# Performance work log

Measured on AMD Instinct MI355X. Metric: run time of the kernel, lower is better.

The kernel has to match this reference:

```python
import jax, jax.numpy as jnp
import numpy as np

EMBED_DIM = 1024
NUM_HEADS = 16
HEAD_DIM = EMBED_DIM // NUM_HEADS
SCALE = HEAD_DIM ** -0.5


def setup_inputs() -> dict:
    key = jax.random.key(0)
    ks = jax.random.split(key, 9)
    B, N = 2, 2048
    s = EMBED_DIM ** -0.5  # ~ torch Linear init scale
    x = jax.random.normal(ks[0], (B, N, EMBED_DIM), dtype=jnp.float32)
    Wq = jax.random.uniform(ks[1], (EMBED_DIM, EMBED_DIM), jnp.float32, -s, s)
    bq = jax.random.uniform(ks[2], (EMBED_DIM,), jnp.float32, -s, s)
    Wk = jax.random.uniform(ks[3], (EMBED_DIM, EMBED_DIM), jnp.float32, -s, s)
    bk = jax.random.uniform(ks[4], (EMBED_DIM,), jnp.float32, -s, s)
    Wv = jax.random.uniform(ks[5], (EMBED_DIM, EMBED_DIM), jnp.float32, -s, s)
    bv = jax.random.uniform(ks[6], (EMBED_DIM,), jnp.float32, -s, s)
    Wo = jax.random.uniform(ks[7], (EMBED_DIM, EMBED_DIM), jnp.float32, -s, s)
    bo = jax.random.uniform(ks[8], (EMBED_DIM,), jnp.float32, -s, s)
    return {"x": x, "Wq": Wq, "bq": bq, "Wk": Wk, "bk": bk,
            "Wv": Wv, "bv": bv, "Wo": Wo, "bo": bo}


def reference(x, Wq, bq, Wk, bk, Wv, bv, Wo, bo):
    B, N, R = x.shape
    H, D = NUM_HEADS, HEAD_DIM
    # projections: Linear(x) = x @ W^T + b; reshape to (B, H, N, D)
    def proj(W, b):
        return (x @ W.T + b).reshape(B, N, H, D).transpose(0, 2, 1, 3)
    q = proj(Wq, bq)
    k = proj(Wk, bk)
    v = proj(Wv, bv)
    attn = jnp.einsum('bhnd,bhmd->bhnm', q, k) * SCALE  # (B,H,N,N)
    attn = jax.nn.softmax(attn, axis=-1)
    out = jnp.einsum('bhnm,bhmd->bhnd', attn, v)        # (B,H,N,D)
    out = out.transpose(0, 2, 1, 3).reshape(B, N, R)
    return out @ Wo.T + bo
```

## Files before the change

kernel.cpp:

```cpp
#include <hip/hip_runtime.h>
#include <stdint.h>

typedef __bf16 bf16;
typedef __bf16 bf16x4 __attribute__((ext_vector_type(4)));
typedef __bf16 bf16x8 __attribute__((ext_vector_type(8)));
typedef float f32x4 __attribute__((ext_vector_type(4)));

#define MFMA16(a, b, c) __builtin_amdgcn_mfma_f32_16x16x32_bf16((a), (b), (c), 0, 0, 0)

#define EMBED 1024
#define SEQ   2048
#define MROWS 4096
#define ATTN_QSCALE 0.1803368801111f

__device__ __forceinline__ void gl2lds16(const bf16* g, bf16* l) {
    __builtin_amdgcn_global_load_lds(
        (const __attribute__((address_space(1))) void*)g,
        (__attribute__((address_space(3))) void*)l,
        16, 0, 0);
}

__global__ __launch_bounds__(256) void cast_all_kernel(
    const float* __restrict__ x,  const float* __restrict__ Wq,
    const float* __restrict__ Wk, const float* __restrict__ Wv,
    const float* __restrict__ Wo, bf16* __restrict__ dst) {
    const int blk = blockIdx.x;
    const float* src;
    size_t so, dofs;
    if (blk < 2048) {
        src = x; so = (size_t)blk * 2048; dofs = so;
    } else {
        const int w = (blk - 2048) >> 9;
        so  = (size_t)((blk - 2048) & 511) * 2048;
        src = (w == 0) ? Wq : (w == 1) ? Wk : (w == 2) ? Wv : Wo;
        dofs = (size_t)(4 + w) * 1024 * 1024 + so;
    }
    const size_t i = (size_t)threadIdx.x * 8;
    float4 a = *(const float4*)(src + so + i);
    float4 b = *(const float4*)(src + so + i + 4);
    bf16x8 o;
    o[0] = (bf16)a.x; o[1] = (bf16)a.y; o[2] = (bf16)a.z; o[3] = (bf16)a.w;
    o[4] = (bf16)b.x; o[5] = (bf16)b.y; o[6] = (bf16)b.z; o[7] = (bf16)b.w;
    *(bf16x8*)(dst + dofs + i) = o;
}

template <bool SCALE>
__device__ __forceinline__ void gemm_tile(const bf16* __restrict__ A,
                                          const bf16* __restrict__ W,
                                          const float* __restrict__ bias,
                                          bf16* __restrict__ C,
                                          int m0, int n0, bf16* smem) {
    const int lane = threadIdx.x & 63;
    const int wv   = threadIdx.x >> 6;
    const int wm   = (wv >> 1) * 64;
    const int wn   = (wv & 1) * 64;
    const int fr   = lane & 15;
    const int quad = lane >> 4;
    const int srow = wv * 8 + (lane >> 3);
    const int swz  = (((lane & 7) ^ ((lane >> 3) & 7))) * 8;

    f32x4 acc[4][4];
#pragma unroll
    for (int mt = 0; mt < 4; ++mt)
#pragma unroll
        for (int nt = 0; nt < 4; ++nt)
            acc[mt][nt] = (f32x4){0.f, 0.f, 0.f, 0.f};

    auto stage = [&](int kt, int bb) {
        bf16* As = smem + bb * 16384;
        bf16* Bs = As + 8192;
        const int k0 = kt * 64;
#pragma unroll
        for (int i = 0; i < 4; ++i) {
            gl2lds16(A + (size_t)(m0 + i * 32 + srow) * 1024 + k0 + swz,
                     &As[(i * 32 + wv * 8) * 64]);
            gl2lds16(W + (size_t)(n0 + i * 32 + srow) * 1024 + k0 + swz,
                     &Bs[(i * 32 + wv * 8) * 64]);
        }
    };

    stage(0, 0);
#pragma unroll
    for (int kt = 0; kt < 16; ++kt) {
        const int bb = kt & 1;
        asm volatile("s_waitcnt vmcnt(0)" ::: "memory");
        __builtin_amdgcn_s_barrier();
        if (kt < 15) stage(kt + 1, bb ^ 1);
        const bf16* As = smem + bb * 16384;
        const bf16* Bs = As + 8192;
#pragma unroll
        for (int ks = 0; ks < 2; ++ks) {
            const int fcol = ((ks * 4 + quad) ^ (fr & 7)) * 8;
            bf16x8 af[4], bfr[4];
#pragma unroll
            for (int t = 0; t < 4; ++t) {
                af[t]  = *(const bf16x8*)&As[(wm + t * 16 + fr) * 64 + fcol];
                bfr[t] = *(const bf16x8*)&Bs[(wn + t * 16 + fr) * 64 + fcol];
            }
            __builtin_amdgcn_s_setprio(1);
#pragma unroll
            for (int mt = 0; mt < 4; ++mt)
#pragma unroll
                for (int nt = 0; nt < 4; ++nt)
                    acc[mt][nt] = MFMA16(af[mt], bfr[nt], acc[mt][nt]);
            __builtin_amdgcn_s_setprio(0);
        }
    }

    float bv[4];
#pragma unroll
    for (int nt = 0; nt < 4; ++nt)
        bv[nt] = bias[n0 + wn + nt * 16 + fr];
    const int row4 = quad * 4;
#pragma unroll
    for (int mt = 0; mt < 4; ++mt)
#pragma unroll
        for (int nt = 0; nt < 4; ++nt)
#pragma unroll
            for (int r = 0; r < 4; ++r) {
                int m = m0 + wm + mt * 16 + row4 + r;
                int n = n0 + wn + nt * 16 + fr;
                float v = acc[mt][nt][r] + bv[nt];
                if (SCALE) v *= ATTN_QSCALE;
                C[(size_t)m * 1024 + n] = (bf16)v;
            }
}

__device__ __forceinline__ void v_tile(const bf16* __restrict__ x,
                                       const bf16* __restrict__ Wv,
                                       const float* __restrict__ bias,
                                       bf16* __restrict__ VT,
                                       int m0, int n0, bf16* smem) {
    const int lane = threadIdx.x & 63;
    const int wv   = threadIdx.x >> 6;
    const int wmW  = (wv >> 1) * 64;
    const int wnT  = (wv & 1) * 64;
    const int f    = lane & 15;
    const int quad = lane >> 4;
    const int srow = wv * 8 + (lane >> 3);
    const int swz  = (((lane & 7) ^ ((lane >> 3) & 7))) * 8;

    f32x4 acc[4][4];
#pragma unroll
    for (int mt = 0; mt < 4; ++mt)
#pragma unroll
        for (int nt = 0; nt < 4; ++nt)
            acc[mt][nt] = (f32x4){0.f, 0.f, 0.f, 0.f};

    auto stage = [&](int kt, int bb) {
        bf16* As = smem + bb * 16384;
        bf16* Bs = As + 8192;
        const int k0 = kt * 64;
#pragma unroll
        for (int i = 0; i < 4; ++i) {
            gl2lds16(x  + (size_t)(m0 + i * 32 + srow) * 1024 + k0 + swz,
                     &As[(i * 32 + wv * 8) * 64]);
            gl2lds16(Wv + (size_t)(n0 + i * 32 + srow) * 1024 + k0 + swz,
                     &Bs[(i * 32 + wv * 8) * 64]);
        }
    };

    stage(0, 0);
#pragma unroll
    for (int kt = 0; kt < 16; ++kt) {
        const int bb = kt & 1;
        asm volatile("s_waitcnt vmcnt(0)" ::: "memory");
        __builtin_amdgcn_s_barrier();
        if (kt < 15) stage(kt + 1, bb ^ 1);
        const bf16* As = smem + bb * 16384;
        const bf16* Bs = As + 8192;
#pragma unroll
        for (int ks = 0; ks < 2; ++ks) {
            const int fcol = ((ks * 4 + quad) ^ (f & 7)) * 8;
            bf16x8 wf[4], xf[4];
#pragma unroll
            for (int t = 0; t < 4; ++t) {
                wf[t] = *(const bf16x8*)&Bs[(wmW + t * 16 + f) * 64 + fcol];
                xf[t] = *(const bf16x8*)&As[(wnT + t * 16 + f) * 64 + fcol];
            }
            __builtin_amdgcn_s_setprio(1);
#pragma unroll
            for (int mt = 0; mt < 4; ++mt)
#pragma unroll
                for (int nt = 0; nt < 4; ++nt)
                    acc[mt][nt] = MFMA16(wf[mt], xf[nt], acc[mt][nt]);
            __builtin_amdgcn_s_setprio(0);
        }
    }

    float4 b4[4];
#pragma unroll
    for (int mt = 0; mt < 4; ++mt)
        b4[mt] = *(const float4*)&bias[n0 + wmW + mt * 16 + quad * 4];

    __syncthreads();

#pragma unroll
    for (int mt = 0; mt < 4; ++mt)
#pragma unroll
        for (int nt = 0; nt < 4; ++nt) {
            const int tok = wnT + nt * 16 + f;
#pragma unroll
            for (int r = 0; r < 4; ++r) {
                const float bvr = (r == 0) ? b4[mt].x : (r == 1) ? b4[mt].y
                                : (r == 2) ? b4[mt].z : b4[mt].w;
                smem[(wmW + mt * 16 + quad * 4 + r) * 136 + tok] =
                    (bf16)(acc[mt][nt][r] + bvr);
            }
        }
    __syncthreads();

    const int n_r  = threadIdx.x >> 4;
    const int t8   = (threadIdx.x & 15) * 8;
    const int base = t8 & ~31;
    const int u4   = ((t8 >> 3) & 3) * 4;
    const int bb   = m0 >> 11;
    const int tokg = (m0 & 2047) + t8;
#pragma unroll
    for (int p = 0; p < 8; ++p) {
        const int n_loc = p * 16 + n_r;
        const bf16* row = &smem[n_loc * 136];
        bf16x4 a = *(const bf16x4*)&row[base + u4];
        bf16x4 b = *(const bf16x4*)&row[base + 16 + u4];
        bf16x8 v = {a[0], a[1], a[2], a[3], b[0], b[1], b[2], b[3]};
        *(bf16x8*)&VT[((size_t)(bb * 1024 + n0 + n_loc)) * 2048 + tokg] = v;
    }
}

__global__ __launch_bounds__(256) void qkv_kernel(
    const bf16* __restrict__ x,
    const bf16* __restrict__ Wq, const float* __restrict__ bq,
    const bf16* __restrict__ Wk, const float* __restrict__ bk,
    const bf16* __restrict__ Wv, const float* __restrict__ bv,
    bf16* __restrict__ Q, bf16* __restrict__ K, bf16* __restrict__ VT) {
    __shared__ __align__(16) bf16 smem[32768];
    const int m0    = blockIdx.x * 128;
    const int which = blockIdx.y >> 3;
    const int n0    = (blockIdx.y & 7) * 128;
    if (which == 0)      gemm_tile<true>(x, Wq, bq, Q, m0, n0, smem);
    else if (which == 1) gemm_tile<false>(x, Wk, bk, K, m0, n0, smem);
    else                 v_tile(x, Wv, bv, VT, m0, n0, smem);
}

__global__ __launch_bounds__(256) void oproj_kernel(
    const bf16* __restrict__ A, const bf16* __restrict__ W,
    const float* __restrict__ bias, float* __restrict__ C) {
    const int m0 = blockIdx.x * 128;
    const int n0 = blockIdx.y * 64;

    __shared__ __align__(16) bf16 smem[24576];

    const int lane = threadIdx.x & 63;
    const int wv   = threadIdx.x >> 6;
    const int wm   = (wv >> 1) * 64;
    const int wn   = (wv & 1) * 32;
    const int fr   = lane & 15;
    const int quad = lane >> 4;
    const int srow = wv * 8 + (lane >> 3);
    const int swz  = (((lane & 7) ^ ((lane >> 3) & 7))) * 8;

    f32x4 acc[4][2];
#pragma unroll
    for (int mt = 0; mt < 4; ++mt)
#pragma unroll
        for (int nt = 0; nt < 2; ++nt)
            acc[mt][nt] = (f32x4){0.f, 0.f, 0.f, 0.f};

    auto stage = [&](int kt, int bb) {
        bf16* As = smem + bb * 12288;
        bf16* Bs = As + 8192;
        const int k0 = kt * 64;
#pragma unroll
        for (int i = 0; i < 4; ++i)
            gl2lds16(A + (size_t)(m0 + i * 32 + srow) * 1024 + k0 + swz,
                     &As[(i * 32 + wv * 8) * 64]);
#pragma unroll
        for (int i = 0; i < 2; ++i)
            gl2lds16(W + (size_t)(n0 + i * 32 + srow) * 1024 + k0 + swz,
                     &Bs[(i * 32 + wv * 8) * 64]);
    };

    stage(0, 0);
#pragma unroll
    for (int kt = 0; kt < 16; ++kt) {
        const int bb = kt & 1;
        asm volatile("s_waitcnt vmcnt(0)" ::: "memory");
        __builtin_amdgcn_s_barrier();
        if (kt < 15) stage(kt + 1, bb ^ 1);
        const bf16* As = smem + bb * 12288;
        const bf16* Bs = As + 8192;
#pragma unroll
        for (int ks = 0; ks < 2; ++ks) {
            const int fcol = ((ks * 4 + quad) ^ (fr & 7)) * 8;
            bf16x8 af[4], bfr[2];
#pragma unroll
            for (int t = 0; t < 4; ++t)
                af[t] = *(const bf16x8*)&As[(wm + t * 16 + fr) * 64 + fcol];
#pragma unroll
            for (int t = 0; t < 2; ++t)
                bfr[t] = *(const bf16x8*)&Bs[(wn + t * 16 + fr) * 64 + fcol];
            __builtin_amdgcn_s_setprio(1);
#pragma unroll
            for (int mt = 0; mt < 4; ++mt)
#pragma unroll
                for (int nt = 0; nt < 2; ++nt)
                    acc[mt][nt] = MFMA16(af[mt], bfr[nt], acc[mt][nt]);
            __builtin_amdgcn_s_setprio(0);
        }
    }

    float bv[2];
#pragma unroll
    for (int nt = 0; nt < 2; ++nt)
        bv[nt] = bias[n0 + wn + nt * 16 + fr];
    const int row4 = quad * 4;
#pragma unroll
    for (int mt = 0; mt < 4; ++mt)
#pragma unroll
        for (int nt = 0; nt < 2; ++nt)
#pragma unroll
            for (int r = 0; r < 4; ++r) {
                int m = m0 + wm + mt * 16 + row4 + r;
                int n = n0 + wn + nt * 16 + fr;
                C[(size_t)m * 1024 + n] = acc[mt][nt][r] + bv[nt];
            }
}

__global__ __launch_bounds__(256, 2) void attn_kernel(
    const bf16* __restrict__ Q, const bf16* __restrict__ K,
    const bf16* __restrict__ VT, bf16* __restrict__ Opart,
    float* __restrict__ lpart) {
    const int tid  = threadIdx.x;
    const int lane = tid & 63;
    const int wv   = tid >> 6;
    const int quad = lane >> 4;
    const int f    = lane & 15;
    const int lin  = blockIdx.y * 16 + blockIdx.x;
    const int sw   = (lin & 7) * 64 + (lin >> 3);
    const int qh   = sw & 15;
    const int bh   = sw >> 4;
    const int qt   = qh >> 1;
    const int half = qh & 1;
    const int q0   = qt * 256;
    const int kvb  = half * 1024;
    const int b    = bh >> 4;
    const int h    = bh & 15;

    const bf16* Qp = Q + ((size_t)b * SEQ) * 1024 + (size_t)h * 64;
    const bf16* Kp = K + ((size_t)b * SEQ) * 1024 + (size_t)h * 64;
    const bf16* Vp = VT + ((size_t)(b * 1024 + h * 64)) * 2048;
    bf16*  Op = Opart + (size_t)half * MROWS * 1024
                      + ((size_t)b * SEQ) * 1024 + (size_t)h * 64;
    float* lp = lpart + ((size_t)(half * 2 + b) * 16 + h) * SEQ;

    __shared__ bf16 Ks[4][64 * 64];
    __shared__ bf16 VTs[4][64 * 64];

    bf16x8 qf[4][2];
#pragma unroll
    for (int qg = 0; qg < 4; ++qg) {
        const bf16* qrow = Qp + (size_t)(q0 + wv * 64 + qg * 16 + f) * 1024;
        qf[qg][0] = *(const bf16x8*)(qrow + quad * 8);
        qf[qg][1] = *(const bf16x8*)(qrow + 32 + quad * 8);
    }

    const int srow = wv * 8 + (lane >> 3);
    const int swz  = (((lane & 7) ^ ((lane >> 3) & 7))) * 8;
    auto stageK = [&](int t, int bb) {
        const int kv0 = kvb + t * 64;
#pragma unroll
        for (int i = 0; i < 2; ++i)
            gl2lds16(Kp + (size_t)(kv0 + i * 32 + srow) * 1024 + swz,
                     &Ks[bb][(i * 32 + wv * 8) * 64]);
    };
    auto stageVT = [&](int t, int bb) {
        const int kv0 = kvb + t * 64;
#pragma unroll
        for (int i = 0; i < 2; ++i)
            gl2lds16(Vp + (size_t)(i * 32 + srow) * 2048 + kv0 + swz,
                     &VTs[bb][(i * 32 + wv * 8) * 64]);
    };

    stageK(0, 0); stageVT(0, 0);
    stageK(1, 1); stageVT(1, 1);

    f32x4 oacc[4][4];
#pragma unroll
    for (int qg = 0; qg < 4; ++qg)
#pragma unroll
        for (int t = 0; t < 4; ++t)
            oacc[qg][t] = (f32x4){0.f, 0.f, 0.f, 0.f};
    f32x4 lacc[4];
#pragma unroll
    for (int qg = 0; qg < 4; ++qg)
        lacc[qg] = (f32x4){0.f, 0.f, 0.f, 0.f};
    const bf16x8 ones8 = {(bf16)1.f, (bf16)1.f, (bf16)1.f, (bf16)1.f,
                          (bf16)1.f, (bf16)1.f, (bf16)1.f, (bf16)1.f};
    const f32x4  zero4 = (f32x4){0.f, 0.f, 0.f, 0.f};

    const int fcol0 = (quad ^ (f & 7)) * 8;
    const int fcol1 = ((4 + quad) ^ (f & 7)) * 8;

    bf16x8 pbA[4][2], pbB[4][2];

    asm volatile("s_waitcnt vmcnt(4)" ::: "memory");
    __builtin_amdgcn_s_barrier();
    {
        bf16x8 kf0[4], kf1[4];
#pragma unroll
        for (int t4 = 0; t4 < 4; ++t4) {
            kf0[t4] = *(const bf16x8*)&Ks[0][(t4 * 16 + f) * 64 + fcol0];
            kf1[t4] = *(const bf16x8*)&Ks[0][(t4 * 16 + f) * 64 + fcol1];
        }
#pragma unroll
        for (int qg = 0; qg < 4; ++qg) {
            f32x4 s[4];
            __builtin_amdgcn_s_setprio(1);
#pragma unroll
            for (int t4 = 0; t4 < 4; ++t4) {
                s[t4] = MFMA16(kf0[t4], qf[qg][0], zero4);
                s[t4] = MFMA16(kf1[t4], qf[qg][1], s[t4]);
            }
            __builtin_amdgcn_s_setprio(0);
#pragma unroll
            for (int kt = 0; kt < 2; ++kt) {
#pragma unroll
                for (int r = 0; r < 4; ++r) {
                    pbA[qg][kt][r]     = (bf16)__builtin_amdgcn_exp2f(s[2 * kt][r]);
                    pbA[qg][kt][4 + r] = (bf16)__builtin_amdgcn_exp2f(s[2 * kt + 1][r]);
                }
                lacc[qg] = MFMA16(ones8, pbA[qg][kt], lacc[qg]);
            }
        }
    }

    auto step = [&](int t, bf16x8 (&pbc)[4][2], bf16x8 (&pbn)[4][2],
                    int drain, bool doStage, bool doQK) {
        if (doStage) { stageK(t + 2, (t + 2) & 3); stageVT(t + 2, (t + 2) & 3); }
        if (drain == 4) asm volatile("s_waitcnt vmcnt(4)" ::: "memory");
        else            asm volatile("s_waitcnt vmcnt(0)" ::: "memory");
        __builtin_amdgcn_s_barrier();
        const int bq = (t + 1) & 3;
        const int bp = t & 3;

        bf16x8 kf0[4], kf1[4];
        if (doQK) {
#pragma unroll
            for (int t4 = 0; t4 < 4; ++t4) {
                kf0[t4] = *(const bf16x8*)&Ks[bq][(t4 * 16 + f) * 64 + fcol0];
                kf1[t4] = *(const bf16x8*)&Ks[bq][(t4 * 16 + f) * 64 + fcol1];
            }
        }
#pragma unroll
        for (int u = 0; u < 4; ++u) {
            f32x4 s[4];
            if (doQK) {
                __builtin_amdgcn_s_setprio(1);
#pragma unroll
                for (int t4 = 0; t4 < 4; ++t4) {
                    s[t4] = MFMA16(kf0[t4], qf[u][0], zero4);
                    s[t4] = MFMA16(kf1[t4], qf[u][1], s[t4]);
                }
                __builtin_amdgcn_s_setprio(0);
            }
            __builtin_amdgcn_s_setprio(1);
#pragma unroll
            for (int kt = 0; kt < 2; ++kt) {
                const int pc = ((kt * 4 + quad) ^ (f & 7)) * 8;
                bf16x8 vf = *(const bf16x8*)&VTs[bp][(u * 16 + f) * 64 + pc];
#pragma unroll
                for (int qg = 0; qg < 4; ++qg)
                    oacc[qg][u] = MFMA16(vf, pbc[qg][kt], oacc[qg][u]);
            }
            __builtin_amdgcn_s_setprio(0);
            if (doQK) {
#pragma unroll
                for (int kt = 0; kt < 2; ++kt) {
#pragma unroll
                    for (int r = 0; r < 4; ++r) {
                        pbn[u][kt][r]     = (bf16)__builtin_amdgcn_exp2f(s[2 * kt][r]);
                        pbn[u][kt][4 + r] = (bf16)__builtin_amdgcn_exp2f(s[2 * kt + 1][r]);
                    }
                    lacc[u] = MFMA16(ones8, pbn[u][kt], lacc[u]);
                }
            }
        }
    };

    for (int tt = 0; tt < 14; tt += 2) {
        step(tt,     pbA, pbB, 4, true, true);
        step(tt + 1, pbB, pbA, 4, true, true);
    }
    step(14, pbA, pbB, 0, false, true);
    step(15, pbB, pbA, 0, false, false);

#pragma unroll
    for (int qg = 0; qg < 4; ++qg) {
        const int q = q0 + wv * 64 + qg * 16 + f;
        bf16* orow = Op + (size_t)q * 1024;
#pragma unroll
        for (int dt = 0; dt < 4; ++dt) {
            bf16x4 ov;
#pragma unroll
            for (int r = 0; r < 4; ++r)
                ov[r] = (bf16)oacc[qg][dt][r];
            *(bf16x4*)(orow + dt * 16 + quad * 4) = ov;
        }
        if (quad == 0)
            lp[q] = lacc[qg][0];
    }
}

__global__ __launch_bounds__(256) void combine_kernel(
    const bf16* __restrict__ Opart, const float* __restrict__ lpart,
    bf16* __restrict__ O) {
    const int gid = blockIdx.x * 256 + threadIdx.x;
    const int row = gid >> 7;
    const int c8  = (gid & 127) * 8;
    const int b   = row >> 11;
    const int tok = row & 2047;
    const int h   = c8 >> 6;

    const float l = lpart[((size_t)(0 * 2 + b) * 16 + h) * SEQ + tok]
                  + lpart[((size_t)(1 * 2 + b) * 16 + h) * SEQ + tok];
    const float inv = 1.0f / l;

    const size_t off = (size_t)row * 1024 + c8;
    bf16x8 a = *(const bf16x8*)&Opart[off];
    bf16x8 c = *(const bf16x8*)&Opart[(size_t)MROWS * 1024 + off];
    bf16x8 o;
#pragma unroll
    for (int i = 0; i < 8; ++i)
        o[i] = (bf16)(((float)a[i] + (float)c[i]) * inv);
    *(bf16x8*)&O[off] = o;
}

extern "C" void kernel_launch(void* const* d_in, const int* in_sizes, int n_in,
                              void* d_out, int out_size, void* d_ws, size_t ws_size,
                              hipStream_t stream) {
    const float* x  = (const float*)d_in[0];
    const float* Wq = (const float*)d_in[1];
    const float* bq = (const float*)d_in[2];
    const float* Wk = (const float*)d_in[3];
    const float* bk = (const float*)d_in[4];
    const float* Wv = (const float*)d_in[5];
    const float* bv = (const float*)d_in[6];
    const float* Wo = (const float*)d_in[7];
    const float* bo = (const float*)d_in[8];
    float* out = (float*)d_out;

    bf16* xb    = (bf16*)d_ws;
    bf16* Wqb   = xb   + (size_t)MROWS * 1024;
    bf16* Wkb   = Wqb  + (size_t)1024 * 1024;
    bf16* Wvb   = Wkb  + (size_t)1024 * 1024;
    bf16* Wob   = Wvb  + (size_t)1024 * 1024;
    bf16* Q     = Wob  + (size_t)1024 * 1024;
    bf16* K     = Q    + (size_t)MROWS * 1024;
    bf16* VT    = K    + (size_t)MROWS * 1024;
    bf16* O     = VT   + (size_t)MROWS * 1024;
    bf16* Opart = O    + (size_t)MROWS * 1024;
    float* lpart = (float*)(Opart + (size_t)2 * MROWS * 1024);

    cast_all_kernel<<<4096, 256, 0, stream>>>(x, Wq, Wk, Wv, Wo, xb);

    qkv_kernel<<<dim3(32, 24), 256, 0, stream>>>(xb, Wqb, bq, Wkb, bk, Wvb, bv, Q, K, VT);
    attn_kernel<<<dim3(16, 32), 256, 0, stream>>>(Q, K, VT, Opart, lpart);
    combine_kernel<<<2048, 256, 0, stream>>>(Opart, lpart, O);
    oproj_kernel<<<dim3(32, 16), 256, 0, stream>>>(O, Wob, bo, out);
}
```

Baseline: 175.8 us.

## Switch projection GEMMs to triple-buffered K=32 stages with partial vmcnt waits

The QKV and output-projection GEMMs now stage K in chunks of 32 instead of 64, using a three-slot LDS ring that is prefetched two stages ahead. Waits use a partial vmcnt, so the next stage's loads stay in flight while the current one is consumed, instead of draining all loads each iteration. LDS per block drops, which may allow more resident blocks. The cost is twice as many barriers, and less MFMA work between them, and the XOR swizzle is narrowed to four 16-byte chunks, which may raise LDS bank conflicts.

New measurement: 180.0 us. 1.02x slower.

```diff
diff --git a/kernel.cpp b/kernel.cpp
--- a/kernel.cpp
+++ b/kernel.cpp
@@ -56,8 +56,9 @@
     const int wn   = (wv & 1) * 64;
     const int fr   = lane & 15;
     const int quad = lane >> 4;
-    const int srow = wv * 8 + (lane >> 3);
-    const int swz  = (((lane & 7) ^ ((lane >> 3) & 7))) * 8;
+    const int srow = wv * 16 + (lane >> 2);
+    const int swz  = ((lane & 3) ^ ((lane >> 2) & 3)) * 8;
+    const int fcol = (quad ^ (fr & 3)) * 8;
 
     f32x4 acc[4][4];
 #pragma unroll
@@ -67,44 +68,41 @@
             acc[mt][nt] = (f32x4){0.f, 0.f, 0.f, 0.f};
 
     auto stage = [&](int kt, int bb) {
-        bf16* As = smem + bb * 16384;
-        bf16* Bs = As + 8192;
-        const int k0 = kt * 64;
-#pragma unroll
-        for (int i = 0; i < 4; ++i) {
-            gl2lds16(A + (size_t)(m0 + i * 32 + srow) * 1024 + k0 + swz,
-                     &As[(i * 32 + wv * 8) * 64]);
-            gl2lds16(W + (size_t)(n0 + i * 32 + srow) * 1024 + k0 + swz,
-                     &Bs[(i * 32 + wv * 8) * 64]);
+        bf16* As = smem + bb * 8192;
+        bf16* Bs = As + 4096;
+        const int k0 = kt * 32;
+#pragma unroll
+        for (int c = 0; c < 2; ++c) {
+            gl2lds16(A + (size_t)(m0 + c * 64 + srow) * 1024 + k0 + swz,
+                     &As[(c * 64 + wv * 16) * 32]);
+            gl2lds16(W + (size_t)(n0 + c * 64 + srow) * 1024 + k0 + swz,
+                     &Bs[(c * 64 + wv * 16) * 32]);
         }
     };
 
     stage(0, 0);
-#pragma unroll
-    for (int kt = 0; kt < 16; ++kt) {
-        const int bb = kt & 1;
-        asm volatile("s_waitcnt vmcnt(0)" ::: "memory");
+    stage(1, 1);
+#pragma unroll
+    for (int kt = 0; kt < 32; ++kt) {
+        if (kt < 31) asm volatile("s_waitcnt vmcnt(4)" ::: "memory");
+        else         asm volatile("s_waitcnt vmcnt(0)" ::: "memory");
         __builtin_amdgcn_s_barrier();
-        if (kt < 15) stage(kt + 1, bb ^ 1);
-        const bf16* As = smem + bb * 16384;
-        const bf16* Bs = As + 8192;
-#pragma unroll
-        for (int ks = 0; ks < 2; ++ks) {
-            const int fcol = ((ks * 4 + quad) ^ (fr & 7)) * 8;
-            bf16x8 af[4], bfr[4];
-#pragma unroll
-            for (int t = 0; t < 4; ++t) {
-                af[t]  = *(const bf16x8*)&As[(wm + t * 16 + fr) * 64 + fcol];
-                bfr[t] = *(const bf16x8*)&Bs[(wn + t * 16 + fr) * 64 + fcol];
-            }
-            __builtin_amdgcn_s_setprio(1);
-#pragma unroll
-            for (int mt = 0; mt < 4; ++mt)
-#pragma unroll
-                for (int nt = 0; nt < 4; ++nt)
-                    acc[mt][nt] = MFMA16(af[mt], bfr[nt], acc[mt][nt]);
-            __builtin_amdgcn_s_setprio(0);
-        }
+        if (kt < 30) stage(kt + 2, (kt + 2) % 3);
+        const bf16* As = smem + (kt % 3) * 8192;
+        const bf16* Bs = As + 4096;
+        bf16x8 af[4], bfr[4];
+#pragma unroll
+        for (int t = 0; t < 4; ++t) {
+            af[t]  = *(const bf16x8*)&As[(wm + t * 16 + fr) * 32 + fcol];
+            bfr[t] = *(const bf16x8*)&Bs[(wn + t * 16 + fr) * 32 + fcol];
+        }
+        __builtin_amdgcn_s_setprio(1);
+#pragma unroll
+        for (int mt = 0; mt < 4; ++mt)
+#pragma unroll
+            for (int nt = 0; nt < 4; ++nt)
+                acc[mt][nt] = MFMA16(af[mt], bfr[nt], acc[mt][nt]);
+        __builtin_amdgcn_s_setprio(0);
     }
 
     float bv[4];
@@ -137,8 +135,9 @@
     const int wnT  = (wv & 1) * 64;
     const int f    = lane & 15;
     const int quad = lane >> 4;
-    const int srow = wv * 8 + (lane >> 3);
-    const int swz  = (((lane & 7) ^ ((lane >> 3) & 7))) * 8;
+    const int srow = wv * 16 + (lane >> 2);
+    const int swz  = ((lane & 3) ^ ((lane >> 2) & 3)) * 8;
+    const int fcol = (quad ^ (f & 3)) * 8;
 
     f32x4 acc[4][4];
 #pragma unroll
@@ -148,44 +147,41 @@
             acc[mt][nt] = (f32x4){0.f, 0.f, 0.f, 0.f};
 
     auto stage = [&](int kt, int bb) {
-        bf16* As = smem + bb * 16384;
-        bf16* Bs = As + 8192;
-        const int k0 = kt * 64;
-#pragma unroll
-        for (int i = 0; i < 4; ++i) {
-            gl2lds16(x  + (size_t)(m0 + i * 32 + srow) * 1024 + k0 + swz,
-                     &As[(i * 32 + wv * 8) * 64]);
-            gl2lds16(Wv + (size_t)(n0 + i * 32 + srow) * 1024 + k0 + swz,
-                     &Bs[(i * 32 + wv * 8) * 64]);
+        bf16* As = smem + bb * 8192;
+        bf16* Bs = As + 4096;
+        const int k0 = kt * 32;
+#pragma unroll
+        for (int c = 0; c < 2; ++c) {
+            gl2lds16(x  + (size_t)(m0 + c * 64 + srow) * 1024 + k0 + swz,
+                     &As[(c * 64 + wv * 16) * 32]);
+            gl2lds16(Wv + (size_t)(n0 + c * 64 + srow) * 1024 + k0 + swz,
+                     &Bs[(c * 64 + wv * 16) * 32]);
         }
     };
 
     stage(0, 0);
-#pragma unroll
-    for (int kt = 0; kt < 16; ++kt) {
-        const int bb = kt & 1;
-        asm volatile("s_waitcnt vmcnt(0)" ::: "memory");
+    stage(1, 1);
+#pragma unroll
+    for (int kt = 0; kt < 32; ++kt) {
+        if (kt < 31) asm volatile("s_waitcnt vmcnt(4)" ::: "memory");
+        else         asm volatile("s_waitcnt vmcnt(0)" ::: "memory");
         __builtin_amdgcn_s_barrier();
-        if (kt < 15) stage(kt + 1, bb ^ 1);
-        const bf16* As = smem + bb * 16384;
-        const bf16* Bs = As + 8192;
-#pragma unroll
-        for (int ks = 0; ks < 2; ++ks) {
-            const int fcol = ((ks * 4 + quad) ^ (f & 7)) * 8;
-            bf16x8 wf[4], xf[4];
-#pragma unroll
-            for (int t = 0; t < 4; ++t) {
-                wf[t] = *(const bf16x8*)&Bs[(wmW + t * 16 + f) * 64 + fcol];
-                xf[t] = *(const bf16x8*)&As[(wnT + t * 16 + f) * 64 + fcol];
-            }
-            __builtin_amdgcn_s_setprio(1);
-#pragma unroll
-            for (int mt = 0; mt < 4; ++mt)
-#pragma unroll
-                for (int nt = 0; nt < 4; ++nt)
-                    acc[mt][nt] = MFMA16(wf[mt], xf[nt], acc[mt][nt]);
-            __builtin_amdgcn_s_setprio(0);
-        }
+        if (kt < 30) stage(kt + 2, (kt + 2) % 3);
+        const bf16* As = smem + (kt % 3) * 8192;
+        const bf16* Bs = As + 4096;
+        bf16x8 wf[4], xf[4];
+#pragma unroll
+        for (int t = 0; t < 4; ++t) {
+            wf[t] = *(const bf16x8*)&Bs[(wmW + t * 16 + f) * 32 + fcol];
+            xf[t] = *(const bf16x8*)&As[(wnT + t * 16 + f) * 32 + fcol];
+        }
+        __builtin_amdgcn_s_setprio(1);
+#pragma unroll
+        for (int mt = 0; mt < 4; ++mt)
+#pragma unroll
+            for (int nt = 0; nt < 4; ++nt)
+                acc[mt][nt] = MFMA16(wf[mt], xf[nt], acc[mt][nt]);
+        __builtin_amdgcn_s_setprio(0);
     }
 
     float4 b4[4];
@@ -233,7 +229,7 @@
     const bf16* __restrict__ Wk, const float* __restrict__ bk,
     const bf16* __restrict__ Wv, const float* __restrict__ bv,
     bf16* __restrict__ Q, bf16* __restrict__ K, bf16* __restrict__ VT) {
-    __shared__ __align__(16) bf16 smem[32768];
+    __shared__ __align__(16) bf16 smem[24576];
     const int m0    = blockIdx.x * 128;
     const int which = blockIdx.y >> 3;
     const int n0    = (blockIdx.y & 7) * 128;
@@ -248,7 +244,7 @@
     const int m0 = blockIdx.x * 128;
     const int n0 = blockIdx.y * 64;
 
-    __shared__ __align__(16) bf16 smem[24576];
+    __shared__ __align__(16) bf16 smem[18432];
 
     const int lane = threadIdx.x & 63;
     const int wv   = threadIdx.x >> 6;
@@ -256,8 +252,9 @@
     const int wn   = (wv & 1) * 32;
     const int fr   = lane & 15;
     const int quad = lane >> 4;
-    const int srow = wv * 8 + (lane >> 3);
-    const int swz  = (((lane & 7) ^ ((lane >> 3) & 7))) * 8;
+    const int srow = wv * 16 + (lane >> 2);
+    const int swz  = ((lane & 3) ^ ((lane >> 2) & 3)) * 8;
+    const int fcol = (quad ^ (fr & 3)) * 8;
 
     f32x4 acc[4][2];
 #pragma unroll
@@ -267,46 +264,41 @@
             acc[mt][nt] = (f32x4){0.f, 0.f, 0.f, 0.f};
 
     auto stage = [&](int kt, int bb) {
-        bf16* As = smem + bb * 12288;
-        bf16* Bs = As + 8192;
-        const int k0 = kt * 64;
-#pragma unroll
-        for (int i = 0; i < 4; ++i)
-            gl2lds16(A + (size_t)(m0 + i * 32 + srow) * 1024 + k0 + swz,
-                     &As[(i * 32 + wv * 8) * 64]);
-#pragma unroll
-        for (int i = 0; i < 2; ++i)
-            gl2lds16(W + (size_t)(n0 + i * 32 + srow) * 1024 + k0 + swz,
-                     &Bs[(i * 32 + wv * 8) * 64]);
+        bf16* As = smem + bb * 6144;
+        bf16* Bs = As + 4096;
+        const int k0 = kt * 32;
+#pragma unroll
+        for (int c = 0; c < 2; ++c)
+            gl2lds16(A + (size_t)(m0 + c * 64 + srow) * 1024 + k0 + swz,
+                     &As[(c * 64 + wv * 16) * 32]);
+        gl2lds16(W + (size_t)(n0 + srow) * 1024 + k0 + swz,
+                 &Bs[(wv * 16) * 32]);
     };
 
     stage(0, 0);
-#pragma unroll
-    for (int kt = 0; kt < 16; ++kt) {
-        const int bb = kt & 1;
-        asm volatile("s_waitcnt vmcnt(0)" ::: "memory");
+    stage(1, 1);
+#pragma unroll
+    for (int kt = 0; kt < 32; ++kt) {
+        if (kt < 31) asm volatile("s_waitcnt vmcnt(3)" ::: "memory");
+        else         asm volatile("s_waitcnt vmcnt(0)" ::: "memory");
         __builtin_amdgcn_s_barrier();
-        if (kt < 15) stage(kt + 1, bb ^ 1);
-        const bf16* As = smem + bb * 12288;
-        const bf16* Bs = As + 8192;
-#pragma unroll
-        for (int ks = 0; ks < 2; ++ks) {
-            const int fcol = ((ks * 4 + quad) ^ (fr & 7)) * 8;
-            bf16x8 af[4], bfr[2];
-#pragma unroll
-            for (int t = 0; t < 4; ++t)
-                af[t] = *(const bf16x8*)&As[(wm + t * 16 + fr) * 64 + fcol];
-#pragma unroll
-            for (int t = 0; t < 2; ++t)
-                bfr[t] = *(const bf16x8*)&Bs[(wn + t * 16 + fr) * 64 + fcol];
-            __builtin_amdgcn_s_setprio(1);
-#pragma unroll
-            for (int mt = 0; mt < 4; ++mt)
-#pragma unroll
-                for (int nt = 0; nt < 2; ++nt)
-                    acc[mt][nt] = MFMA16(af[mt], bfr[nt], acc[mt][nt]);
-            __builtin_amdgcn_s_setprio(0);
-        }
+        if (kt < 30) stage(kt + 2, (kt + 2) % 3);
+        const bf16* As = smem + (kt % 3) * 6144;
+        const bf16* Bs = As + 4096;
+        bf16x8 af[4], bfr[2];
+#pragma unroll
+        for (int t = 0; t < 4; ++t)
+            af[t] = *(const bf16x8*)&As[(wm + t * 16 + fr) * 32 + fcol];
+#pragma unroll
+        for (int t = 0; t < 2; ++t)
+            bfr[t] = *(const bf16x8*)&Bs[(wn + t * 16 + fr) * 32 + fcol];
+        __builtin_amdgcn_s_setprio(1);
+#pragma unroll
+        for (int mt = 0; mt < 4; ++mt)
+#pragma unroll
+            for (int nt = 0; nt < 2; ++nt)
+                acc[mt][nt] = MFMA16(af[mt], bfr[nt], acc[mt][nt]);
+        __builtin_amdgcn_s_setprio(0);
     }
 
     float bv[2];
```
